# Optimization experiments

Hardware: AMD Instinct MI355X
Metric: run time of the kernel (lower is better)

## Reference

```python
import jax, jax.numpy as jnp
import numpy as np

GRID_H, GRID_W = 16, 16
N_NODES = GRID_H * GRID_W
LATENT = 256
N = 65536


def setup_inputs() -> dict:
    key = jax.random.key(0)
    k1, k2 = jax.random.split(key)
    z_e_sample = jax.random.normal(k1, (N, LATENT), dtype=jnp.float32)
    embeddings = jax.random.normal(k2, (N_NODES, LATENT), dtype=jnp.float32) * 0.05
    return {"z_e_sample": z_e_sample, "embeddings": embeddings, "alpha_som": 10}


def _distances_flat(z, e):
    # ||z - e||^2 = ||z||^2 + ||e||^2 - 2 z.e  -> GEMM form instead of
    # materializing the [N, n_nodes, latent] broadcast of the torch chunked loop.
    z2 = jnp.sum(z * z, axis=1, keepdims=True)            # [N, 1]
    e2 = jnp.sum(e * e, axis=1)                           # [n_nodes]
    d = z2 + e2[None, :] - 2.0 * (z @ e.T)                # [N, n_nodes]
    return jnp.maximum(d, 0.0)


def _neighbor_indices(bmu):
    # toroidal 4-neighborhood on the GRID_H x GRID_W SOM grid
    k1 = bmu // GRID_W
    k2 = bmu % GRID_W
    idx_up = ((k1 - 1) % GRID_H) * GRID_W + k2
    idx_down = ((k1 + 1) % GRID_H) * GRID_W + k2
    idx_left = k1 * GRID_W + (k2 - 1) % GRID_W
    idx_right = k1 * GRID_W + (k2 + 1) % GRID_W
    # order matches torch: [self, up, down, right, left]
    return jnp.stack([bmu, idx_up, idx_down, idx_right, idx_left], axis=1)


def reference(z_e_sample, embeddings, alpha_som):
    d = _distances_flat(z_e_sample, embeddings)           # [N, n_nodes]
    bmu = jnp.argmin(d, axis=1)                           # [N]
    z_q = embeddings[bmu]                                 # [N, latent]
    z_q_neighbors = embeddings[_neighbor_indices(bmu)]    # [N, 5, latent]
    a = jnp.float32(alpha_som)
    q = (1.0 / (1.0 + d / a)) ** ((a + 1.0) / 2.0)
    q = q / jnp.sum(q, axis=1, keepdims=True)
    q = q + jnp.finfo(q.dtype).eps                        # [N, n_nodes]
    return z_q, z_q_neighbors, q, bmu
```

## Files before the change

### kernel.cpp

```cpp
#include <hip/hip_runtime.h>
#include <math.h>

#define BM 64
#define BK 32
#define NLAT 256
#define NNOD 256

typedef float f4 __attribute__((ext_vector_type(4)));

__device__ __forceinline__ void gload_lds16(const void* g, void* l) {
  __builtin_amdgcn_global_load_lds((const __attribute__((address_space(1))) void*)g,
                                   (__attribute__((address_space(3))) void*)l, 16, 0, 0);
}

__global__ void prep_kernel(const float* __restrict__ E, float* __restrict__ Et,
                            float* __restrict__ e2) {
  const int n = blockIdx.x;
  const int k = threadIdx.x;
  float v = E[n * NLAT + k];
  Et[k * NNOD + n] = v;
  float s = v * v;
#pragma unroll
  for (int m = 1; m <= 32; m <<= 1) s += __shfl_xor(s, m);
  __shared__ float ws[4];
  if ((threadIdx.x & 63) == 0) ws[threadIdx.x >> 6] = s;
  __syncthreads();
  if (threadIdx.x == 0) e2[n] = ws[0] + ws[1] + ws[2] + ws[3];
}

__launch_bounds__(256, 3)
__global__ void som_kernel(const float* __restrict__ Z, const float* __restrict__ E,
                           const float* __restrict__ Et, const float* __restrict__ e2g,
                           const int* __restrict__ alphap,
                           float* __restrict__ out_zq, float* __restrict__ out_nbr,
                           float* __restrict__ out_q, float* __restrict__ out_bmu) {
  __shared__ float As[BM][BK];
  __shared__ float Bs[BK][NNOD];
  __shared__ float z2s[BM];

  const int tid = threadIdx.x;
  const int lane = tid & 63;
  const int wv = tid >> 6;
  const int tr = tid >> 5;
  const int tc = tid & 31;
  const long brow = (long)blockIdx.x * BM;

  float acc[8][8];
#pragma unroll
  for (int i = 0; i < 8; ++i)
#pragma unroll
    for (int j = 0; j < 8; ++j) acc[i][j] = 0.f;

  float z2p = 0.f;
  const int m2 = tid >> 2;
  const int kq = tid & 3;

#pragma unroll 1
  for (int ks = 0; ks < 8; ++ks) {
    const int k0 = ks * BK;
    __syncthreads();
#pragma unroll
    for (int t = 0; t < 2; ++t) {
      const int q = wv * 2 + t;
      const int m = q * 8 + (lane >> 3);
      const float* src = Z + (brow + m) * NLAT + k0 + (lane & 7) * 4;
      gload_lds16(src, &As[q * 8][0]);
    }
#pragma unroll
    for (int t = 0; t < 8; ++t) {
      const int kk = wv * 8 + t;
      const float* src = Et + (long)(k0 + kk) * NNOD + lane * 4;
      gload_lds16(src, &Bs[kk][0]);
    }
    __syncthreads();
    {
      f4 s0 = *(const f4*)&As[m2][kq * 8];
      f4 s1 = *(const f4*)&As[m2][kq * 8 + 4];
      z2p += s0[0] * s0[0] + s0[1] * s0[1] + s0[2] * s0[2] + s0[3] * s0[3] +
             s1[0] * s1[0] + s1[1] * s1[1] + s1[2] * s1[2] + s1[3] * s1[3];
    }
#pragma unroll
    for (int kb = 0; kb < 8; ++kb) {
      f4 av[8];
#pragma unroll
      for (int i = 0; i < 8; ++i) av[i] = *(const f4*)&As[tr * 8 + i][kb * 4];
#pragma unroll
      for (int kk = 0; kk < 4; ++kk) {
        f4 b0 = *(const f4*)&Bs[kb * 4 + kk][tc * 8];
        f4 b1 = *(const f4*)&Bs[kb * 4 + kk][tc * 8 + 4];
#pragma unroll
        for (int i = 0; i < 8; ++i) {
          const float a = av[i][kk];
          acc[i][0] = fmaf(a, b0[0], acc[i][0]);
          acc[i][1] = fmaf(a, b0[1], acc[i][1]);
          acc[i][2] = fmaf(a, b0[2], acc[i][2]);
          acc[i][3] = fmaf(a, b0[3], acc[i][3]);
          acc[i][4] = fmaf(a, b1[0], acc[i][4]);
          acc[i][5] = fmaf(a, b1[1], acc[i][5]);
          acc[i][6] = fmaf(a, b1[2], acc[i][6]);
          acc[i][7] = fmaf(a, b1[3], acc[i][7]);
        }
      }
    }
  }

  z2p += __shfl_xor(z2p, 1);
  z2p += __shfl_xor(z2p, 2);
  if (kq == 0) z2s[m2] = z2p;
  __syncthreads();

  const float alpha = (float)(*alphap);
  const float ex = (alpha + 1.f) * 0.5f;
  const float ra = 1.f / alpha;
  f4 e2a = *(const f4*)&e2g[tc * 8];
  f4 e2b = *(const f4*)&e2g[tc * 8 + 4];
  float e2r[8] = {e2a[0], e2a[1], e2a[2], e2a[3], e2b[0], e2b[1], e2b[2], e2b[3]};

#pragma unroll 1
  for (int i = 0; i < 8; ++i) {
    const int rloc = tr * 8 + i;
    const long row = brow + rloc;
    const float z2 = z2s[rloc];
    float d[8];
#pragma unroll
    for (int j = 0; j < 8; ++j)
      d[j] = fmaxf(z2 + e2r[j] - 2.f * acc[i][j], 0.f);
    float dm = d[0];
    int im = tc * 8;
#pragma unroll
    for (int j = 1; j < 8; ++j) {
      if (d[j] < dm) { dm = d[j]; im = tc * 8 + j; }
    }
#pragma unroll
    for (int m = 1; m <= 16; m <<= 1) {
      float od = __shfl_xor(dm, m);
      int oi = __shfl_xor(im, m);
      if (od < dm || (od == dm && oi < im)) { dm = od; im = oi; }
    }
    float qv[8];
    float qs = 0.f;
#pragma unroll
    for (int j = 0; j < 8; ++j) {
      float u = 1.f / (1.f + d[j] * ra);
      qv[j] = __expf(ex * __logf(u));
      qs += qv[j];
    }
#pragma unroll
    for (int m = 1; m <= 16; m <<= 1) qs += __shfl_xor(qs, m);
    const float ri = 1.f / qs;
    f4 q0, q1;
#pragma unroll
    for (int j = 0; j < 4; ++j) {
      q0[j] = qv[j] * ri + 1.1920929e-7f;
      q1[j] = qv[j + 4] * ri + 1.1920929e-7f;
    }
    *(f4*)&out_q[row * NNOD + tc * 8] = q0;
    *(f4*)&out_q[row * NNOD + tc * 8 + 4] = q1;

    const int bmu = im;
    if (tc == 0) out_bmu[row] = (float)bmu;

    const int k1 = bmu >> 4, k2 = bmu & 15;
    int nidx[5];
    nidx[0] = bmu;
    nidx[1] = ((k1 + 15) & 15) * 16 + k2;
    nidx[2] = ((k1 + 1) & 15) * 16 + k2;
    nidx[3] = (k1 << 4) + ((k2 + 1) & 15);
    nidx[4] = (k1 << 4) + ((k2 + 15) & 15);
#pragma unroll
    for (int nb = 0; nb < 5; ++nb) {
      f4 v0 = *(const f4*)&E[nidx[nb] * NLAT + tc * 8];
      f4 v1 = *(const f4*)&E[nidx[nb] * NLAT + tc * 8 + 4];
      *(f4*)&out_nbr[(row * 5 + nb) * NLAT + tc * 8] = v0;
      *(f4*)&out_nbr[(row * 5 + nb) * NLAT + tc * 8 + 4] = v1;
      if (nb == 0) {
        *(f4*)&out_zq[row * NLAT + tc * 8] = v0;
        *(f4*)&out_zq[row * NLAT + tc * 8 + 4] = v1;
      }
    }
  }
}

extern "C" void kernel_launch(void* const* d_in, const int* in_sizes, int n_in,
                              void* d_out, int out_size, void* d_ws, size_t ws_size,
                              hipStream_t stream) {
  const float* Z = (const float*)d_in[0];
  const float* E = (const float*)d_in[1];
  const int* alphap = (const int*)d_in[2];
  const long N = (long)in_sizes[0] / NLAT;

  float* Et = (float*)d_ws;
  float* e2 = (float*)((char*)d_ws + NLAT * NNOD * 4);

  float* out = (float*)d_out;
  float* out_zq = out;
  float* out_nbr = out + N * NLAT;
  float* out_q = out + N * NLAT + N * 5 * NLAT;
  float* out_bmu = out + N * NLAT * 2 + N * 5 * NLAT;

  prep_kernel<<<NNOD, 256, 0, stream>>>(E, Et, e2);
  som_kernel<<<(int)(N / BM), 256, 0, stream>>>(Z, E, Et, e2, alphap,
                                                out_zq, out_nbr, out_q, out_bmu);
}
```

Before: 702.6 us.

## Shrink K tile, split column mapping, use nontemporal stores and coalesced BMU writes

Halves the K tile to cut LDS use and raises the launch-bounds occupancy target from 3 to 4 blocks. Each thread now owns two 4-wide column groups, 128 columns apart, instead of 8 contiguous columns, which changes the LDS B reads and the global store pattern. Output stores become nontemporal so the large write stream does not pollute the caches. BMU values are staged in shared memory and written as one coalesced store per block. The risks are more loop iterations and barriers per K, and register pressure from the tighter launch bound.

```diff
diff --git a/kernel.cpp b/kernel.cpp
--- a/kernel.cpp
+++ b/kernel.cpp
@@ -2,7 +2,7 @@
 #include <math.h>
 
 #define BM 64
-#define BK 32
+#define BK 16
 #define NLAT 256
 #define NNOD 256
 
@@ -28,7 +28,7 @@
   if (threadIdx.x == 0) e2[n] = ws[0] + ws[1] + ws[2] + ws[3];
 }
 
-__launch_bounds__(256, 3)
+__launch_bounds__(256, 4)
 __global__ void som_kernel(const float* __restrict__ Z, const float* __restrict__ E,
                            const float* __restrict__ Et, const float* __restrict__ e2g,
                            const int* __restrict__ alphap,
@@ -37,6 +37,7 @@
   __shared__ float As[BM][BK];
   __shared__ float Bs[BK][NNOD];
   __shared__ float z2s[BM];
+  __shared__ float bmus[BM];
 
   const int tid = threadIdx.x;
   const int lane = tid & 63;
@@ -45,6 +46,9 @@
   const int tc = tid & 31;
   const long brow = (long)blockIdx.x * BM;
 
+  const int c0 = tc * 4;
+  const int c1 = 128 + tc * 4;
+
   float acc[8][8];
 #pragma unroll
   for (int i = 0; i < 8; ++i)
@@ -56,38 +60,33 @@
   const int kq = tid & 3;
 
 #pragma unroll 1
-  for (int ks = 0; ks < 8; ++ks) {
+  for (int ks = 0; ks < NLAT / BK; ++ks) {
     const int k0 = ks * BK;
     __syncthreads();
-#pragma unroll
-    for (int t = 0; t < 2; ++t) {
-      const int q = wv * 2 + t;
-      const int m = q * 8 + (lane >> 3);
-      const float* src = Z + (brow + m) * NLAT + k0 + (lane & 7) * 4;
-      gload_lds16(src, &As[q * 8][0]);
-    }
-#pragma unroll
-    for (int t = 0; t < 8; ++t) {
-      const int kk = wv * 8 + t;
+    {
+      const float* src = Z + (brow + wv * 16 + (lane >> 2)) * NLAT + k0 + (lane & 3) * 4;
+      gload_lds16(src, &As[wv * 16][0]);
+    }
+#pragma unroll
+    for (int t = 0; t < 4; ++t) {
+      const int kk = wv * 4 + t;
       const float* src = Et + (long)(k0 + kk) * NNOD + lane * 4;
       gload_lds16(src, &Bs[kk][0]);
     }
     __syncthreads();
     {
-      f4 s0 = *(const f4*)&As[m2][kq * 8];
-      f4 s1 = *(const f4*)&As[m2][kq * 8 + 4];
-      z2p += s0[0] * s0[0] + s0[1] * s0[1] + s0[2] * s0[2] + s0[3] * s0[3] +
-             s1[0] * s1[0] + s1[1] * s1[1] + s1[2] * s1[2] + s1[3] * s1[3];
-    }
-#pragma unroll
-    for (int kb = 0; kb < 8; ++kb) {
+      f4 s0 = *(const f4*)&As[m2][kq * 4];
+      z2p += s0[0] * s0[0] + s0[1] * s0[1] + s0[2] * s0[2] + s0[3] * s0[3];
+    }
+#pragma unroll
+    for (int kb = 0; kb < BK / 4; ++kb) {
       f4 av[8];
 #pragma unroll
       for (int i = 0; i < 8; ++i) av[i] = *(const f4*)&As[tr * 8 + i][kb * 4];
 #pragma unroll
       for (int kk = 0; kk < 4; ++kk) {
-        f4 b0 = *(const f4*)&Bs[kb * 4 + kk][tc * 8];
-        f4 b1 = *(const f4*)&Bs[kb * 4 + kk][tc * 8 + 4];
+        f4 b0 = *(const f4*)&Bs[kb * 4 + kk][c0];
+        f4 b1 = *(const f4*)&Bs[kb * 4 + kk][c1];
 #pragma unroll
         for (int i = 0; i < 8; ++i) {
           const float a = av[i][kk];
@@ -112,8 +111,8 @@
   const float alpha = (float)(*alphap);
   const float ex = (alpha + 1.f) * 0.5f;
   const float ra = 1.f / alpha;
-  f4 e2a = *(const f4*)&e2g[tc * 8];
-  f4 e2b = *(const f4*)&e2g[tc * 8 + 4];
+  f4 e2a = *(const f4*)&e2g[c0];
+  f4 e2b = *(const f4*)&e2g[c1];
   float e2r[8] = {e2a[0], e2a[1], e2a[2], e2a[3], e2b[0], e2b[1], e2b[2], e2b[3]};
 
 #pragma unroll 1
@@ -126,10 +125,11 @@
     for (int j = 0; j < 8; ++j)
       d[j] = fmaxf(z2 + e2r[j] - 2.f * acc[i][j], 0.f);
     float dm = d[0];
-    int im = tc * 8;
+    int im = c0;
 #pragma unroll
     for (int j = 1; j < 8; ++j) {
-      if (d[j] < dm) { dm = d[j]; im = tc * 8 + j; }
+      const int col = (j < 4) ? (c0 + j) : (c1 + j - 4);
+      if (d[j] < dm) { dm = d[j]; im = col; }
     }
 #pragma unroll
     for (int m = 1; m <= 16; m <<= 1) {
@@ -154,11 +154,11 @@
       q0[j] = qv[j] * ri + 1.1920929e-7f;
       q1[j] = qv[j + 4] * ri + 1.1920929e-7f;
     }
-    *(f4*)&out_q[row * NNOD + tc * 8] = q0;
-    *(f4*)&out_q[row * NNOD + tc * 8 + 4] = q1;
+    __builtin_nontemporal_store(q0, (f4*)&out_q[row * NNOD + c0]);
+    __builtin_nontemporal_store(q1, (f4*)&out_q[row * NNOD + c1]);
 
     const int bmu = im;
-    if (tc == 0) out_bmu[row] = (float)bmu;
+    if (tc == 0) bmus[rloc] = (float)bmu;
 
     const int k1 = bmu >> 4, k2 = bmu & 15;
     int nidx[5];
@@ -169,16 +169,19 @@
     nidx[4] = (k1 << 4) + ((k2 + 15) & 15);
 #pragma unroll
     for (int nb = 0; nb < 5; ++nb) {
-      f4 v0 = *(const f4*)&E[nidx[nb] * NLAT + tc * 8];
-      f4 v1 = *(const f4*)&E[nidx[nb] * NLAT + tc * 8 + 4];
-      *(f4*)&out_nbr[(row * 5 + nb) * NLAT + tc * 8] = v0;
-      *(f4*)&out_nbr[(row * 5 + nb) * NLAT + tc * 8 + 4] = v1;
+      f4 v0 = *(const f4*)&E[nidx[nb] * NLAT + c0];
+      f4 v1 = *(const f4*)&E[nidx[nb] * NLAT + c1];
+      __builtin_nontemporal_store(v0, (f4*)&out_nbr[(row * 5 + nb) * NLAT + c0]);
+      __builtin_nontemporal_store(v1, (f4*)&out_nbr[(row * 5 + nb) * NLAT + c1]);
       if (nb == 0) {
-        *(f4*)&out_zq[row * NLAT + tc * 8] = v0;
-        *(f4*)&out_zq[row * NLAT + tc * 8 + 4] = v1;
+        __builtin_nontemporal_store(v0, (f4*)&out_zq[row * NLAT + c0]);
+        __builtin_nontemporal_store(v1, (f4*)&out_zq[row * NLAT + c1]);
       }
     }
   }
+
+  __syncthreads();
+  if (tid < BM) out_bmu[brow + tid] = bmus[tid];
 }
 
 extern "C" void kernel_launch(void* const* d_in, const int* in_sizes, int n_in,
```

After: 776.6 us. +10.5%, slower.
